# Performance work log

Hardware: AMD Instinct MI355X
Metric: run time of the kernel (lower is better)

Reference implementation:

```python
import jax, jax.numpy as jnp
import numpy as np

B, S, H, DH, DE, DC = 32, 1024, 2, 64, 128, 64  # batch, seq, heads, dim_head, dim_emb, dim_ctx


def setup_inputs() -> dict:
    key = jax.random.key(0)
    ks = jax.random.split(key, 16)
    p = lambda k, shp: (jax.random.normal(k, shp, dtype=jnp.float32) * 0.02)
    return {
        "queries_it": jax.random.normal(ks[0], (B, S, DE), dtype=jnp.float32),
        "queries_ctx": jax.random.normal(ks[1], (B, S, DC), dtype=jnp.float32),
        "keys_it": jax.random.normal(ks[2], (B, S, DE), dtype=jnp.float32),
        "keys_ctx": jax.random.normal(ks[3], (B, S, DC), dtype=jnp.float32),
        "sigma_noise": jax.random.uniform(ks[4], (B, H), dtype=jnp.float32),
        "noise": jax.random.normal(ks[5], (B, 2, S, S), dtype=jnp.float32),
        "Wq_it": p(ks[6], (DH, DE)), "bq_it": jnp.zeros((DH,), jnp.float32),
        "Wk_it": p(ks[7], (DH, DE)), "bk_it": jnp.zeros((DH,), jnp.float32),
        "Wq_ctx": p(ks[8], (DH, DC)), "bq_ctx": jnp.zeros((DH,), jnp.float32),
        "Wk_ctx": p(ks[9], (DH, DC)), "bk_ctx": jnp.zeros((DH,), jnp.float32),
        "Wv": p(ks[10], (DE, DE)), "bv": jnp.zeros((DE,), jnp.float32),
        "W1": p(ks[11], (H, 2)), "b1": jnp.zeros((H,), jnp.float32),
        "W2": p(ks[12], (H, H)), "b2": jnp.zeros((H,), jnp.float32),
    }


def reference(queries_it, queries_ctx, keys_it, keys_ctx, sigma_noise, noise,
              Wq_it, bq_it, Wk_it, bk_it, Wq_ctx, bq_ctx, Wk_ctx, bk_ctx,
              Wv, bv, W1, b1, W2, b2):
    # dual QK projections
    Q_it = queries_it @ Wq_it.T + bq_it          # [B,Sq,DH]
    K_it = keys_it @ Wk_it.T + bk_it             # [B,Sk,DH]
    Q_ctx = queries_ctx @ Wq_ctx.T + bq_ctx
    K_ctx = keys_ctx @ Wk_ctx.T + bk_ctx
    s_it = jnp.einsum('bqd,bkd->bqk', Q_it, K_it)
    s_ctx = jnp.einsum('bqd,bkd->bqk', Q_ctx, K_ctx)
    scores = jnp.stack([s_it, s_ctx], axis=1)    # [B,2,Sq,Sk]
    # additive per-head noise (sigma viewed [B,H,1,1], H==2)
    scores = scores + noise * (sigma_noise[:, :, None, None] ** 2)
    # per-element HDP MLP: 2 -> H -> H over last axis
    x = jnp.transpose(scores, (0, 2, 3, 1))      # [B,Sq,Sk,2]
    h = jax.nn.relu(x @ W1.T + b1)
    s = h @ W2.T + b2                            # [B,Sq,Sk,H]
    s = jnp.transpose(s, (0, 3, 1, 2)) / (DH ** 0.5)  # [B,H,Sq,Sk]
    # key padding mask
    key_mask = jnp.sign(jnp.sum(jnp.abs(keys_it), axis=-1))      # [B,Sk]
    s = jnp.where(key_mask[:, None, None, :] == 0, -1e9, s)
    att = jax.nn.softmax(s, axis=-1)
    # query padding mask (applied after softmax, as in the original)
    query_mask = jnp.sign(jnp.sum(jnp.abs(queries_it), axis=-1))  # [B,Sq]
    att = att * query_mask[:, None, :, None]
    # values
    V = (keys_it @ Wv.T + bv).reshape(B, S, H, DH)               # [B,Sk,H,DH]
    out = jnp.einsum('bhqk,bkhd->bqhd', att, V).reshape(B, S, H * DH)
    return out + queries_it
```

## Files before the change

### kernel.cpp

```cpp
#include <hip/hip_runtime.h>

#define B_N 32
#define S_N 1024

typedef __attribute__((ext_vector_type(8))) short sh8;
typedef __attribute__((ext_vector_type(4))) short sh4;
typedef __attribute__((ext_vector_type(4))) float f4;

#define AS1 __attribute__((address_space(1)))
#define AS3 __attribute__((address_space(3)))

__device__ __forceinline__ short f2bf(float f) {
  unsigned u = __builtin_bit_cast(unsigned, f);
  u += 0x7fff + ((u >> 16) & 1);
  return (short)(u >> 16);
}

#if defined(__has_builtin)
#if __has_builtin(__builtin_amdgcn_mfma_f32_16x16x16bf16_1k)
#define HAVE_MFMA16 1
#endif
#endif
__device__ __forceinline__ f4 mfma16(sh4 a, sh4 b, f4 c) {
#ifdef HAVE_MFMA16
  return __builtin_amdgcn_mfma_f32_16x16x16bf16_1k(a, b, c, 0, 0, 0);
#else
  asm volatile("v_mfma_f32_16x16x16_bf16 %0, %1, %2, %0\n\ts_nop 7\n\ts_nop 7"
               : "+v"(c) : "v"(a), "v"(b));
  return c;
#endif
}

__device__ __forceinline__ sh8 cvt8(const float* src, float& s) {
  f4 x0 = *(const f4*)src;
  f4 x1 = *(const f4*)(src + 4);
  sh8 v;
#pragma unroll
  for (int i = 0; i < 4; ++i) {
    v[i] = f2bf(x0[i]);
    v[4 + i] = f2bf(x1[i]);
    s += fabsf(x0[i]) + fabsf(x1[i]);
  }
  return v;
}

template <int DIN, bool MASK>
__device__ __forceinline__ void dev_proj(
    const float* __restrict__ in, const float* __restrict__ W,
    const float* __restrict__ bias, short* __restrict__ out,
    float* __restrict__ mask, int blk) {
  constexpr int NSL = DIN / 8;
  constexpr int KT = DIN / 32;
  __shared__ __align__(16) short a_t[128 * DIN];
  __shared__ __align__(16) short w_t[64 * DIN];
  const int tid = threadIdx.x;
  const int wave = tid >> 6, lane = tid & 63;
  const int col = lane & 15, grp = lane >> 4;
  const size_t r0g = (size_t)blk * 128;

#pragma unroll
  for (int t = 0; t < 128 * NSL / 256; ++t) {
    const int u = t * 256 + tid, row = u / NSL, sl = u % NSL;
    float s = 0.f;
    sh8 v = cvt8(in + (r0g + row) * DIN + sl * 8, s);
    *(sh8*)&a_t[(row * NSL + (sl ^ (row & (NSL - 1)))) * 8] = v;
    if (MASK) {
      s += __shfl_xor(s, 1); s += __shfl_xor(s, 2);
      s += __shfl_xor(s, 4); s += __shfl_xor(s, 8);
      if ((lane & 15) == 0) mask[r0g + row] = (s != 0.f) ? 1.f : 0.f;
    }
  }
#pragma unroll
  for (int t = 0; t < 64 * NSL / 256; ++t) {
    const int u = t * 256 + tid, row = u / NSL, sl = u % NSL;
    float s = 0.f;
    sh8 v = cvt8(W + (size_t)row * DIN + sl * 8, s);
    *(sh8*)&w_t[(row * NSL + (sl ^ (row & (NSL - 1)))) * 8] = v;
  }
  __syncthreads();

  const int r0 = wave * 32;
  sh8 a[2][KT];
#pragma unroll
  for (int ri = 0; ri < 2; ++ri)
#pragma unroll
    for (int t = 0; t < KT; ++t) {
      const int row = r0 + ri * 16 + col;
      a[ri][t] = *(const sh8*)&a_t[(row * NSL + ((grp + 4 * t) ^ (row & (NSL - 1)))) * 8];
    }
  f4 acc[2][4];
#pragma unroll
  for (int ri = 0; ri < 2; ++ri)
#pragma unroll
    for (int jt = 0; jt < 4; ++jt) acc[ri][jt] = (f4)0.f;
#pragma unroll
  for (int jt = 0; jt < 4; ++jt) {
    const int j = jt * 16 + col;
    sh8 bw[KT];
#pragma unroll
    for (int t = 0; t < KT; ++t)
      bw[t] = *(const sh8*)&w_t[(j * NSL + ((grp + 4 * t) ^ (j & (NSL - 1)))) * 8];
#pragma unroll
    for (int ri = 0; ri < 2; ++ri)
#pragma unroll
      for (int t = 0; t < KT; ++t)
        acc[ri][jt] = __builtin_amdgcn_mfma_f32_16x16x32_bf16(a[ri][t], bw[t], acc[ri][jt], 0, 0, 0);
  }
#pragma unroll
  for (int jt = 0; jt < 4; ++jt) {
    const float bj = bias[jt * 16 + col];
#pragma unroll
    for (int ri = 0; ri < 2; ++ri)
#pragma unroll
      for (int r = 0; r < 4; ++r)
        out[(r0g + r0 + ri * 16 + grp * 4 + r) * 64 + jt * 16 + col] = f2bf(acc[ri][jt][r] + bj);
  }
}

__global__ __launch_bounds__(256) void proj_q_kernel(
    const float* __restrict__ in, const float* __restrict__ W,
    const float* __restrict__ bias, short* __restrict__ out,
    float* __restrict__ mask) {
  dev_proj<128, true>(in, W, bias, out, mask, blockIdx.x);
}

__global__ __launch_bounds__(256) void proj_ctx2_kernel(
    const float* __restrict__ in0, const float* __restrict__ W0,
    const float* __restrict__ b0, short* __restrict__ o0,
    const float* __restrict__ in1, const float* __restrict__ W1_,
    const float* __restrict__ b1_, short* __restrict__ o1, int nb) {
  const int sel = blockIdx.x >= nb;
  const int blk = sel ? (blockIdx.x - nb) : blockIdx.x;
  dev_proj<64, false>(sel ? in1 : in0, sel ? W1_ : W0, sel ? b1_ : b0,
                      sel ? o1 : o0, nullptr, blk);
}

__global__ __launch_bounds__(256) void proj_k_mfma(
    const float* __restrict__ in, const float* __restrict__ Wk, const float* __restrict__ bk_,
    const float* __restrict__ Wv, const float* __restrict__ bv_,
    short* __restrict__ kit, short* __restrict__ vt, float* __restrict__ km) {
  __shared__ __align__(16) char ulds[65536];
  short* a_t = (short*)ulds;
  short* w_t = (short*)(ulds + 32768);
  const int tid = threadIdx.x;
  const int wave = tid >> 6, lane = tid & 63;
  const int col = lane & 15, grp = lane >> 4;
  const size_t r0g = (size_t)blockIdx.x * 128;
  const int bb = (int)(r0g >> 10), s0 = (int)(r0g & 1023);

#pragma unroll
  for (int t = 0; t < 8; ++t) {
    const int u = t * 256 + tid, row = u >> 4, sl = u & 15;
    float s = 0.f;
    sh8 v = cvt8(in + (r0g + row) * 128 + sl * 8, s);
    *(sh8*)&a_t[(row * 16 + (sl ^ (row & 15))) * 8] = v;
    s += __shfl_xor(s, 1); s += __shfl_xor(s, 2);
    s += __shfl_xor(s, 4); s += __shfl_xor(s, 8);
    if ((lane & 15) == 0) km[r0g + row] = (s != 0.f) ? 1.f : 0.f;
  }
#pragma unroll
  for (int t = 0; t < 8; ++t) {
    const int u = t * 256 + tid, row = u >> 4, sl = u & 15;
    const float* src = (row < 64) ? (Wk + (size_t)row * 128) : (Wv + (size_t)(row - 64) * 128);
    float s = 0.f;
    sh8 v = cvt8(src + sl * 8, s);
    *(sh8*)&w_t[(row * 16 + (sl ^ (row & 15))) * 8] = v;
  }
  __syncthreads();

  const int r0 = wave * 32;
  sh8 a[2][4];
#pragma unroll
  for (int ri = 0; ri < 2; ++ri)
#pragma unroll
    for (int t = 0; t < 4; ++t) {
      const int row = r0 + ri * 16 + col;
      a[ri][t] = *(const sh8*)&a_t[(row * 16 + ((grp + 4 * t) ^ (row & 15))) * 8];
    }
  f4 acck[2][4], accv[2][8];
#pragma unroll
  for (int ri = 0; ri < 2; ++ri) {
#pragma unroll
    for (int jt = 0; jt < 4; ++jt) acck[ri][jt] = (f4)0.f;
#pragma unroll
    for (int jt = 0; jt < 8; ++jt) accv[ri][jt] = (f4)0.f;
  }
#pragma unroll
  for (int jt = 0; jt < 8; ++jt) {
    const int j = jt * 16 + col;
    sh8 bw[4];
#pragma unroll
    for (int t = 0; t < 4; ++t)
      bw[t] = *(const sh8*)&w_t[(j * 16 + ((grp + 4 * t) ^ (j & 15))) * 8];
#pragma unroll
    for (int ri = 0; ri < 2; ++ri)
#pragma unroll
      for (int t = 0; t < 4; ++t) {
        f4& dst = (jt < 4) ? acck[ri][jt] : accv[ri][jt - 4];
        dst = __builtin_amdgcn_mfma_f32_16x16x32_bf16(a[ri][t], bw[t], dst, 0, 0, 0);
      }
  }
#pragma unroll
  for (int jt = 0; jt < 4; ++jt) {
    const float bj = bk_[jt * 16 + col];
#pragma unroll
    for (int ri = 0; ri < 2; ++ri)
#pragma unroll
      for (int r = 0; r < 4; ++r)
        kit[(r0g + r0 + ri * 16 + grp * 4 + r) * 64 + jt * 16 + col] = f2bf(acck[ri][jt][r] + bj);
  }
  __syncthreads();
#pragma unroll
  for (int t = 0; t < 4; ++t) {
    const int u = t * 256 + tid, row = u >> 4, sl = u & 15;
    float s = 0.f;
    sh8 v = cvt8(Wv + (size_t)(64 + row) * 128 + sl * 8, s);
    *(sh8*)&w_t[(row * 16 + (sl ^ (row & 15))) * 8] = v;
  }
  __syncthreads();
#pragma unroll
  for (int jt = 0; jt < 4; ++jt) {
    const int j = jt * 16 + col;
    sh8 bw[4];
#pragma unroll
    for (int t = 0; t < 4; ++t)
      bw[t] = *(const sh8*)&w_t[(j * 16 + ((grp + 4 * t) ^ (j & 15))) * 8];
#pragma unroll
    for (int ri = 0; ri < 2; ++ri)
#pragma unroll
      for (int t = 0; t < 4; ++t)
        accv[ri][4 + jt] = __builtin_amdgcn_mfma_f32_16x16x32_bf16(a[ri][t], bw[t], accv[ri][4 + jt], 0, 0, 0);
  }
  __syncthreads();
  short* vtile = (short*)ulds;
#pragma unroll
  for (int vjt = 0; vjt < 8; ++vjt) {
    const int j = vjt * 16 + col;
    const float bvj = bv_[j];
#pragma unroll
    for (int ri = 0; ri < 2; ++ri)
#pragma unroll
      for (int r = 0; r < 4; ++r)
        vtile[j * 136 + r0 + ri * 16 + grp * 4 + r] = f2bf(accv[ri][vjt][r] + bvj);
  }
  __syncthreads();
  const int j2 = tid >> 1, half = tid & 1;
  short* dst = vt + ((size_t)(bb * 128 + j2)) * S_N + s0 + half * 64;
#pragma unroll
  for (int i = 0; i < 8; ++i)
    *(sh8*)(dst + i * 8) = *(const sh8*)&vtile[j2 * 136 + half * 64 + i * 8];
}

__global__ __launch_bounds__(256, 2) void attn_kernel(
    const short* __restrict__ qit, const short* __restrict__ kit,
    const short* __restrict__ qctx, const short* __restrict__ kctx,
    const short* __restrict__ vt,
    const float* __restrict__ noise,
    const float* __restrict__ sigma,
    const float* __restrict__ qmask, const float* __restrict__ kmask,
    const float* __restrict__ qin,
    const float* __restrict__ W1, const float* __restrict__ b1,
    const float* __restrict__ W2, const float* __restrict__ b2,
    float* __restrict__ out) {
  __shared__ __align__(16) char bufs[4][16384];
  __shared__ float kml[1024];
  __shared__ float lsum_lds[4][2][16];

  const int tid = threadIdx.x;
  const int wave = tid >> 6, lane = tid & 63;
  const int bid = blockIdx.x;
  const int wg = ((bid & 7) << 6) | (bid >> 3);
  const int b = wg >> 4, qt = wg & 15;
  const int qblk = qt * 64;
  const int qbase = qblk + wave * 16;
  const int col = lane & 15, grp = lane >> 4;
  const int swk = col & 7;

  const float w100 = W1[0], w101 = W1[1], w110 = W1[2], w111 = W1[3];
  const float bb10 = b1[0], bb11 = b1[1];
  const float sc = 0.125f;
  const float w200 = W2[0] * sc, w201 = W2[1] * sc, w210 = W2[2] * sc, w211 = W2[3] * sc;
  const float bb20 = b2[0] * sc, bb21 = b2[1] * sc;
  float sg0 = sigma[b * 2 + 0]; sg0 *= sg0;
  float sg1 = sigma[b * 2 + 1]; sg1 *= sg1;

  const int qrow = qbase + col;
  sh8 aqit[2], aqctx[2];
#pragma unroll
  for (int t = 0; t < 2; ++t) {
    aqit[t] = *(const sh8*)(qit + ((size_t)(b * S_N + qrow)) * 64 + grp * 8 + t * 32);
    aqctx[t] = *(const sh8*)(qctx + ((size_t)(b * S_N + qrow)) * 64 + grp * 8 + t * 32);
  }

  f4 acc[2][4];
#pragma unroll
  for (int h = 0; h < 2; ++h)
#pragma unroll
    for (int dt = 0; dt < 4; ++dt) acc[h][dt] = (f4)0.f;
  float rs0 = 0.f, rs1 = 0.f;

  const float* nz_g = noise + (size_t)(b * 2) * S_N * S_N;
  const short* kit_g = kit + (size_t)b * S_N * 64;
  const short* kctx_g = kctx + (size_t)b * S_N * 64;
  const short* vt_g = vt + (size_t)b * 128 * S_N;

  for (int i = tid; i < 1024; i += 256) kml[i] = kmask[(size_t)b * S_N + i];
  __syncthreads();

  auto STAGE = [&](char* buf, int kc) {
    if (wave == 0) {
#pragma unroll
      for (int j = 0; j < 2; ++j) {
        const int u = j * 64 + lane, row = u >> 3, sl = u & 7;
        const size_t off = (size_t)(kc + row) * 64 + ((sl ^ (row & 7)) << 3);
        __builtin_amdgcn_global_load_lds((const AS1 unsigned*)(kit_g + off),
                                         (AS3 unsigned*)(buf + j * 1024), 16, 0, 0);
      }
    } else if (wave == 1) {
#pragma unroll
      for (int j = 0; j < 2; ++j) {
        const int u = j * 64 + lane, row = u >> 3, sl = u & 7;
        const size_t off = (size_t)(kc + row) * 64 + ((sl ^ (row & 7)) << 3);
        __builtin_amdgcn_global_load_lds((const AS1 unsigned*)(kctx_g + off),
                                         (AS3 unsigned*)(buf + 2048 + j * 1024), 16, 0, 0);
      }
    } else {
#pragma unroll
      for (int i = 0; i < 2; ++i) {
        const int un = (wave - 2) * 2 + i;
        const int u = un * 64 + lane, d = u >> 1, sl = u & 1;
        const short* g = vt_g + (size_t)d * S_N + kc + ((sl ^ (d & 1)) << 3);
        __builtin_amdgcn_global_load_lds((const AS1 unsigned*)g,
                                         (AS3 unsigned*)(buf + 4096 + un * 1024), 16, 0, 0);
      }
    }
#pragma unroll
    for (int h = 0; h < 2; ++h) {
      const int q = lane >> 2, sg = lane & 3, jq = sg ^ (q & 3);
      const float* g = nz_g + (size_t)h * S_N * S_N + (size_t)(qbase + q) * S_N + kc + jq * 4;
      __builtin_amdgcn_global_load_lds((const AS1 unsigned*)g,
                                       (AS3 unsigned*)(buf + 8192 + wave * 2048 + h * 1024), 16, 0, 0);
    }
  };

  STAGE(bufs[0], 0);
  STAGE(bufs[1], 16);
  STAGE(bufs[2], 32);

#pragma unroll 1
  for (int k = 0; k < 64; ++k) {
    asm volatile("s_waitcnt vmcnt(10)" ::: "memory");
    __builtin_amdgcn_sched_barrier(0);
    __builtin_amdgcn_s_barrier();
    STAGE(bufs[(k + 3) & 3], ((k + 3) & 63) * 16);

    const char* cur = bufs[k & 3];
    const short* Kb = (const short*)cur;
    const short* Cb = (const short*)(cur + 2048);
    const short* Vb = (const short*)(cur + 4096);

    f4 sit = (f4)0.f, sctx = (f4)0.f;
#pragma unroll
    for (int t = 0; t < 2; ++t) {
      const int so = ((grp + 4 * t) ^ swk) * 8;
      sh8 bk = *(const sh8*)&Kb[col * 64 + so];
      sit = __builtin_amdgcn_mfma_f32_16x16x32_bf16(bk, aqit[t], sit, 0, 0, 0);
      sh8 bc = *(const sh8*)&Cb[col * 64 + so];
      sctx = __builtin_amdgcn_mfma_f32_16x16x32_bf16(bc, aqctx[t], sctx, 0, 0, 0);
    }
    asm volatile("s_waitcnt vmcnt(12)" ::: "memory");
    __builtin_amdgcn_sched_barrier(0);
    const float* Nw = (const float*)(cur + 8192 + wave * 2048);
    const int jq = grp ^ (col & 3);
    f4 n0 = *(const f4*)&Nw[col * 16 + jq * 4];
    f4 n1 = *(const f4*)&Nw[256 + col * 16 + jq * 4];
    f4 km = *(const f4*)&kml[k * 16 + grp * 4];
    sh4 po, pc;
#pragma unroll
    for (int r = 0; r < 4; ++r) {
      float x0 = fmaf(n0[r], sg0, sit[r]);
      float x1 = fmaf(n1[r], sg1, sctx[r]);
      float h0 = fmaxf(fmaf(w101, x1, fmaf(w100, x0, bb10)), 0.f);
      float h1 = fmaxf(fmaf(w111, x1, fmaf(w110, x0, bb11)), 0.f);
      float L0 = fmaf(w201, h1, fmaf(w200, h0, bb20));
      float L1 = fmaf(w211, h1, fmaf(w210, h0, bb21));
      float p0 = __expf(L0) * km[r];
      float p1 = __expf(L1) * km[r];
      rs0 += p0;
      rs1 += p1;
      po[r] = f2bf(p0);
      pc[r] = f2bf(p1);
    }
#pragma unroll
    for (int h = 0; h < 2; ++h) {
      const sh4 pa = h ? pc : po;
#pragma unroll
      for (int dt = 0; dt < 4; ++dt) {
        const int drow = h * 64 + dt * 16 + col;
        const int phys = (grp >> 1) ^ (drow & 1);
        sh4 bv = *(const sh4*)&Vb[drow * 16 + phys * 8 + (grp & 1) * 4];
        acc[h][dt] = mfma16(pa, bv, acc[h][dt]);
      }
    }
  }

  rs0 += __shfl_xor(rs0, 16); rs0 += __shfl_xor(rs0, 32);
  rs1 += __shfl_xor(rs1, 16); rs1 += __shfl_xor(rs1, 32);
  if (lane < 16) {
    lsum_lds[wave][0][col] = rs0;
    lsum_lds[wave][1][col] = rs1;
  }
  __syncthreads();
  f4 ls0 = *(const f4*)&lsum_lds[wave][0][grp * 4];
  f4 ls1 = *(const f4*)&lsum_lds[wave][1][grp * 4];
  f4 qm4 = *(const f4*)(qmask + (size_t)b * S_N + qbase + grp * 4);
#pragma unroll
  for (int h = 0; h < 2; ++h)
#pragma unroll
    for (int dt = 0; dt < 4; ++dt)
#pragma unroll
      for (int r = 0; r < 4; ++r) {
        const float s2 = qm4[r] / (h ? ls1[r] : ls0[r]);
        const size_t o = ((size_t)(b * S_N + qbase + grp * 4 + r)) * 128 + h * 64 + dt * 16 + col;
        out[o] = acc[h][dt][r] * s2 + qin[o];
      }
}

extern "C" void kernel_launch(void* const* d_in, const int* in_sizes, int n_in,
                              void* d_out, int out_size, void* d_ws, size_t ws_size,
                              hipStream_t stream) {
  const float* queries_it = (const float*)d_in[0];
  const float* queries_ctx = (const float*)d_in[1];
  const float* keys_it = (const float*)d_in[2];
  const float* keys_ctx = (const float*)d_in[3];
  const float* sigma = (const float*)d_in[4];
  const float* noise = (const float*)d_in[5];
  const float* Wq_it = (const float*)d_in[6];
  const float* bq_it = (const float*)d_in[7];
  const float* Wk_it = (const float*)d_in[8];
  const float* bk_it = (const float*)d_in[9];
  const float* Wq_ctx = (const float*)d_in[10];
  const float* bq_ctx = (const float*)d_in[11];
  const float* Wk_ctx = (const float*)d_in[12];
  const float* bk_ctx = (const float*)d_in[13];
  const float* Wv = (const float*)d_in[14];
  const float* bv = (const float*)d_in[15];
  const float* W1 = (const float*)d_in[16];
  const float* b1 = (const float*)d_in[17];
  const float* W2 = (const float*)d_in[18];
  const float* b2 = (const float*)d_in[19];
  float* out = (float*)d_out;

  char* ws = (char*)d_ws;
  short* qit = (short*)(ws);
  short* kit = (short*)(ws + (4ull << 20));
  short* qctx = (short*)(ws + (8ull << 20));
  short* kctx = (short*)(ws + (12ull << 20));
  short* vt = (short*)(ws + (16ull << 20));
  float* qmask = (float*)(ws + (24ull << 20));
  float* kmask = (float*)(ws + (24ull << 20) + (size_t)B_N * S_N * 4);

  const int NB = B_N * S_N / 128;
  proj_q_kernel<<<dim3(NB), 256, 0, stream>>>(queries_it, Wq_it, bq_it, qit, qmask);
  proj_k_mfma<<<dim3(NB), 256, 0, stream>>>(keys_it, Wk_it, bk_it, Wv, bv, kit, vt, kmask);
  proj_ctx2_kernel<<<dim3(2 * NB), 256, 0, stream>>>(
      queries_ctx, Wq_ctx, bq_ctx, qctx, keys_ctx, Wk_ctx, bk_ctx, kctx, NB);

  attn_kernel<<<dim3(B_N * (S_N / 64)), 256, 0, stream>>>(
      qit, kit, qctx, kctx, vt, noise, sigma, qmask, kmask, queries_it,
      W1, b1, W2, b2, out);
}
```

Baseline: 131.3 us.

## Process 64-key chunks with double buffering and 16x16x32 MFMA for PV

The attention loop now handles 64 keys per iteration instead of 16, double-buffering 64KB LDS stages in place of a four-deep ring of 16KB stages. This cuts barrier and wait overhead per key. The probabilities are written to a per-wave LDS scratch tile and read back as 8-wide operands, so P*V can use the 16x16x32 bf16 MFMA instead of 16x16x16. LDS use grows to about 150KB, which drops occupancy to one block per CU (launch bounds relaxed accordingly) and adds an LDS round-trip for P.

```diff
diff --git a/kernel.cpp b/kernel.cpp
--- a/kernel.cpp
+++ b/kernel.cpp
@@ -14,21 +14,6 @@
   unsigned u = __builtin_bit_cast(unsigned, f);
   u += 0x7fff + ((u >> 16) & 1);
   return (short)(u >> 16);
-}
-
-#if defined(__has_builtin)
-#if __has_builtin(__builtin_amdgcn_mfma_f32_16x16x16bf16_1k)
-#define HAVE_MFMA16 1
-#endif
-#endif
-__device__ __forceinline__ f4 mfma16(sh4 a, sh4 b, f4 c) {
-#ifdef HAVE_MFMA16
-  return __builtin_amdgcn_mfma_f32_16x16x16bf16_1k(a, b, c, 0, 0, 0);
-#else
-  asm volatile("v_mfma_f32_16x16x16_bf16 %0, %1, %2, %0\n\ts_nop 7\n\ts_nop 7"
-               : "+v"(c) : "v"(a), "v"(b));
-  return c;
-#endif
 }
 
 __device__ __forceinline__ sh8 cvt8(const float* src, float& s) {
@@ -251,7 +236,7 @@
     *(sh8*)(dst + i * 8) = *(const sh8*)&vtile[j2 * 136 + half * 64 + i * 8];
 }
 
-__global__ __launch_bounds__(256, 2) void attn_kernel(
+__global__ __launch_bounds__(256) void attn_kernel(
     const short* __restrict__ qit, const short* __restrict__ kit,
     const short* __restrict__ qctx, const short* __restrict__ kctx,
     const short* __restrict__ vt,
@@ -262,9 +247,9 @@
     const float* __restrict__ W1, const float* __restrict__ b1,
     const float* __restrict__ W2, const float* __restrict__ b2,
     float* __restrict__ out) {
-  __shared__ __align__(16) char bufs[4][16384];
-  __shared__ float kml[1024];
-  __shared__ float lsum_lds[4][2][16];
+  __shared__ __align__(16) char lds_all[2 * 65536 + 16384 + 4096 + 512];
+  float* kml = (float*)(lds_all + 2 * 65536 + 16384);
+  float* lsum = (float*)(lds_all + 2 * 65536 + 16384 + 4096);
 
   const int tid = threadIdx.x;
   const int wave = tid >> 6, lane = tid & 63;
@@ -303,103 +288,129 @@
   const short* kit_g = kit + (size_t)b * S_N * 64;
   const short* kctx_g = kctx + (size_t)b * S_N * 64;
   const short* vt_g = vt + (size_t)b * 128 * S_N;
+  short* Pw = (short*)(lds_all + 2 * 65536 + wave * 4096);
 
   for (int i = tid; i < 1024; i += 256) kml[i] = kmask[(size_t)b * S_N + i];
   __syncthreads();
 
-  auto STAGE = [&](char* buf, int kc) {
+  auto STAGE_KV = [&](char* buf, int kc) {
     if (wave == 0) {
 #pragma unroll
-      for (int j = 0; j < 2; ++j) {
-        const int u = j * 64 + lane, row = u >> 3, sl = u & 7;
-        const size_t off = (size_t)(kc + row) * 64 + ((sl ^ (row & 7)) << 3);
-        __builtin_amdgcn_global_load_lds((const AS1 unsigned*)(kit_g + off),
-                                         (AS3 unsigned*)(buf + j * 1024), 16, 0, 0);
+      for (int i = 0; i < 8; ++i) {
+        const int idx = i * 64 + lane, row = idx >> 3, sl = idx & 7;
+        const short* g = kit_g + (size_t)(kc + row) * 64 + ((sl ^ (row & 7)) << 3);
+        __builtin_amdgcn_global_load_lds((const AS1 unsigned*)g,
+                                         (AS3 unsigned*)(buf + i * 1024), 16, 0, 0);
       }
     } else if (wave == 1) {
 #pragma unroll
-      for (int j = 0; j < 2; ++j) {
-        const int u = j * 64 + lane, row = u >> 3, sl = u & 7;
-        const size_t off = (size_t)(kc + row) * 64 + ((sl ^ (row & 7)) << 3);
-        __builtin_amdgcn_global_load_lds((const AS1 unsigned*)(kctx_g + off),
-                                         (AS3 unsigned*)(buf + 2048 + j * 1024), 16, 0, 0);
+      for (int i = 0; i < 8; ++i) {
+        const int idx = i * 64 + lane, row = idx >> 3, sl = idx & 7;
+        const short* g = kctx_g + (size_t)(kc + row) * 64 + ((sl ^ (row & 7)) << 3);
+        __builtin_amdgcn_global_load_lds((const AS1 unsigned*)g,
+                                         (AS3 unsigned*)(buf + 8192 + i * 1024), 16, 0, 0);
       }
     } else {
 #pragma unroll
-      for (int i = 0; i < 2; ++i) {
-        const int un = (wave - 2) * 2 + i;
-        const int u = un * 64 + lane, d = u >> 1, sl = u & 1;
-        const short* g = vt_g + (size_t)d * S_N + kc + ((sl ^ (d & 1)) << 3);
+      for (int i = 0; i < 8; ++i) {
+        const int vi = (wave - 2) * 8 + i;
+        const int idx = vi * 64 + lane, d = idx >> 3, sl = idx & 7;
+        const short* g = vt_g + (size_t)d * S_N + kc + ((sl ^ (d & 7)) << 3);
         __builtin_amdgcn_global_load_lds((const AS1 unsigned*)g,
-                                         (AS3 unsigned*)(buf + 4096 + un * 1024), 16, 0, 0);
-      }
-    }
-#pragma unroll
-    for (int h = 0; h < 2; ++h) {
-      const int q = lane >> 2, sg = lane & 3, jq = sg ^ (q & 3);
-      const float* g = nz_g + (size_t)h * S_N * S_N + (size_t)(qbase + q) * S_N + kc + jq * 4;
+                                         (AS3 unsigned*)(buf + 16384 + vi * 1024), 16, 0, 0);
+      }
+    }
+  };
+  auto STAGE_N = [&](char* buf, int kc) {
+#pragma unroll
+    for (int i = 0; i < 8; ++i) {
+      const int idx = i * 64 + lane;
+      const int head = idx >> 8, q = (idx >> 4) & 15, phi = idx & 15;
+      const int j = phi ^ q;
+      const float* g = nz_g + (size_t)head * S_N * S_N + (size_t)(qbase + q) * S_N + kc + j * 4;
       __builtin_amdgcn_global_load_lds((const AS1 unsigned*)g,
-                                       (AS3 unsigned*)(buf + 8192 + wave * 2048 + h * 1024), 16, 0, 0);
+                                       (AS3 unsigned*)(buf + 32768 + wave * 8192 + i * 1024), 16, 0, 0);
     }
   };
 
-  STAGE(bufs[0], 0);
-  STAGE(bufs[1], 16);
-  STAGE(bufs[2], 32);
+  STAGE_KV(lds_all, 0);
+  STAGE_N(lds_all, 0);
 
 #pragma unroll 1
-  for (int k = 0; k < 64; ++k) {
-    asm volatile("s_waitcnt vmcnt(10)" ::: "memory");
+  for (int k = 0; k < 16; ++k) {
+    char* cur = lds_all + (size_t)(k & 1) * 65536;
+    char* nxt = lds_all + (size_t)((k + 1) & 1) * 65536;
+    const int kc = k * 64;
+    asm volatile("s_waitcnt vmcnt(8)" ::: "memory");
     __builtin_amdgcn_sched_barrier(0);
     __builtin_amdgcn_s_barrier();
-    STAGE(bufs[(k + 3) & 3], ((k + 3) & 63) * 16);
-
-    const char* cur = bufs[k & 3];
+    {
+      const int kc2 = ((k + 1) & 15) * 64;
+      STAGE_KV(nxt, kc2);
+      STAGE_N(nxt, kc2);
+    }
+
     const short* Kb = (const short*)cur;
-    const short* Cb = (const short*)(cur + 2048);
-    const short* Vb = (const short*)(cur + 4096);
-
-    f4 sit = (f4)0.f, sctx = (f4)0.f;
-#pragma unroll
-    for (int t = 0; t < 2; ++t) {
-      const int so = ((grp + 4 * t) ^ swk) * 8;
-      sh8 bk = *(const sh8*)&Kb[col * 64 + so];
-      sit = __builtin_amdgcn_mfma_f32_16x16x32_bf16(bk, aqit[t], sit, 0, 0, 0);
-      sh8 bc = *(const sh8*)&Cb[col * 64 + so];
-      sctx = __builtin_amdgcn_mfma_f32_16x16x32_bf16(bc, aqctx[t], sctx, 0, 0, 0);
-    }
-    asm volatile("s_waitcnt vmcnt(12)" ::: "memory");
+    const short* Cb = (const short*)(cur + 8192);
+    const short* Vb = (const short*)(cur + 16384);
+    const float* Nw = (const float*)(cur + 32768 + wave * 8192);
+
+    f4 sit[4], sctx[4];
+#pragma unroll
+    for (int kt = 0; kt < 4; ++kt) {
+      const int krow = kt * 16 + col;
+      sit[kt] = (f4)0.f;
+      sctx[kt] = (f4)0.f;
+#pragma unroll
+      for (int t = 0; t < 2; ++t) {
+        const int so = ((grp + 4 * t) ^ swk) * 8;
+        sh8 bk = *(const sh8*)&Kb[krow * 64 + so];
+        sit[kt] = __builtin_amdgcn_mfma_f32_16x16x32_bf16(bk, aqit[t], sit[kt], 0, 0, 0);
+        sh8 bc = *(const sh8*)&Cb[krow * 64 + so];
+        sctx[kt] = __builtin_amdgcn_mfma_f32_16x16x32_bf16(bc, aqctx[t], sctx[kt], 0, 0, 0);
+      }
+    }
+    asm volatile("s_waitcnt vmcnt(16)" ::: "memory");
     __builtin_amdgcn_sched_barrier(0);
-    const float* Nw = (const float*)(cur + 8192 + wave * 2048);
-    const int jq = grp ^ (col & 3);
-    f4 n0 = *(const f4*)&Nw[col * 16 + jq * 4];
-    f4 n1 = *(const f4*)&Nw[256 + col * 16 + jq * 4];
-    f4 km = *(const f4*)&kml[k * 16 + grp * 4];
-    sh4 po, pc;
-#pragma unroll
-    for (int r = 0; r < 4; ++r) {
-      float x0 = fmaf(n0[r], sg0, sit[r]);
-      float x1 = fmaf(n1[r], sg1, sctx[r]);
-      float h0 = fmaxf(fmaf(w101, x1, fmaf(w100, x0, bb10)), 0.f);
-      float h1 = fmaxf(fmaf(w111, x1, fmaf(w110, x0, bb11)), 0.f);
-      float L0 = fmaf(w201, h1, fmaf(w200, h0, bb20));
-      float L1 = fmaf(w211, h1, fmaf(w210, h0, bb21));
-      float p0 = __expf(L0) * km[r];
-      float p1 = __expf(L1) * km[r];
-      rs0 += p0;
-      rs1 += p1;
-      po[r] = f2bf(p0);
-      pc[r] = f2bf(p1);
+
+#pragma unroll
+    for (int kt = 0; kt < 4; ++kt) {
+      const int phi = (kt * 4 + grp) ^ col;
+      f4 n0 = *(const f4*)&Nw[col * 64 + phi * 4];
+      f4 n1 = *(const f4*)&Nw[1024 + col * 64 + phi * 4];
+      f4 km = *(const f4*)&kml[kc + kt * 16 + grp * 4];
+      sh4 po, pc;
+#pragma unroll
+      for (int r = 0; r < 4; ++r) {
+        float x0 = fmaf(n0[r], sg0, sit[kt][r]);
+        float x1 = fmaf(n1[r], sg1, sctx[kt][r]);
+        float h0 = fmaxf(fmaf(w101, x1, fmaf(w100, x0, bb10)), 0.f);
+        float h1 = fmaxf(fmaf(w111, x1, fmaf(w110, x0, bb11)), 0.f);
+        float L0 = fmaf(w201, h1, fmaf(w200, h0, bb20));
+        float L1 = fmaf(w211, h1, fmaf(w210, h0, bb21));
+        float p0 = __expf(L0) * km[r];
+        float p1 = __expf(L1) * km[r];
+        rs0 += p0;
+        rs1 += p1;
+        po[r] = f2bf(p0);
+        pc[r] = f2bf(p1);
+      }
+      const int so = ((kt * 2 + (grp >> 1)) ^ swk) * 8 + (grp & 1) * 4;
+      *(sh4*)&Pw[col * 64 + so] = po;
+      *(sh4*)&Pw[1024 + col * 64 + so] = pc;
     }
 #pragma unroll
     for (int h = 0; h < 2; ++h) {
-      const sh4 pa = h ? pc : po;
-#pragma unroll
-      for (int dt = 0; dt < 4; ++dt) {
-        const int drow = h * 64 + dt * 16 + col;
-        const int phys = (grp >> 1) ^ (drow & 1);
-        sh4 bv = *(const sh4*)&Vb[drow * 16 + phys * 8 + (grp & 1) * 4];
-        acc[h][dt] = mfma16(pa, bv, acc[h][dt]);
+#pragma unroll
+      for (int t = 0; t < 2; ++t) {
+        const int so = ((grp + 4 * t) ^ swk) * 8;
+        sh8 pa = *(const sh8*)&Pw[h * 1024 + col * 64 + so];
+#pragma unroll
+        for (int dt = 0; dt < 4; ++dt) {
+          const int drow = h * 64 + dt * 16 + col;
+          sh8 bv = *(const sh8*)&Vb[drow * 64 + so];
+          acc[h][dt] = __builtin_amdgcn_mfma_f32_16x16x32_bf16(pa, bv, acc[h][dt], 0, 0, 0);
+        }
       }
     }
   }
@@ -407,12 +418,12 @@
   rs0 += __shfl_xor(rs0, 16); rs0 += __shfl_xor(rs0, 32);
   rs1 += __shfl_xor(rs1, 16); rs1 += __shfl_xor(rs1, 32);
   if (lane < 16) {
-    lsum_lds[wave][0][col] = rs0;
-    lsum_lds[wave][1][col] = rs1;
-  }
-  __syncthreads();
-  f4 ls0 = *(const f4*)&lsum_lds[wave][0][grp * 4];
-  f4 ls1 = *(const f4*)&lsum_lds[wave][1][grp * 4];
+    lsum[(wave * 2 + 0) * 16 + col] = rs0;
+    lsum[(wave * 2 + 1) * 16 + col] = rs1;
+  }
+  __syncthreads();
+  f4 ls0 = *(const f4*)&lsum[(wave * 2 + 0) * 16 + grp * 4];
+  f4 ls1 = *(const f4*)&lsum[(wave * 2 + 1) * 16 + grp * 4];
   f4 qm4 = *(const f4*)(qmask + (size_t)b * S_N + qbase + grp * 4);
 #pragma unroll
   for (int h = 0; h < 2; ++h)
```

New measurement: 119.4 us. 9.1% less time.
